# Kernel tuning notes

Hardware: AMD Instinct MI355X
Metric: run time of the kernel (lower is better)

The kernel has to match this reference:

```python
import jax, jax.numpy as jnp
import numpy as np

EMB_DIM = 1024
NUM_HEADS = 16
HEAD_DIM = EMB_DIM // NUM_HEADS
SEQ_LEN = 2048
BATCH = 2


def setup_inputs() -> dict:
    key = jax.random.key(0)
    k1, k2, k3 = jax.random.split(key, 3)
    scale = 1.0 / np.sqrt(EMB_DIM)
    x = jax.random.normal(k1, (BATCH, SEQ_LEN, EMB_DIM), dtype=jnp.float32)
    w_qkv = jax.random.normal(k2, (EMB_DIM, 3 * EMB_DIM), dtype=jnp.float32) * scale
    w_proj = jax.random.normal(k3, (EMB_DIM, EMB_DIM), dtype=jnp.float32) * scale
    b_proj = jnp.zeros((EMB_DIM,), dtype=jnp.float32)
    return {"x": x, "w_qkv": w_qkv, "w_proj": w_proj, "b_proj": b_proj}


def reference(x, w_qkv, w_proj, b_proj):
    B, T, E = x.shape
    qkv = x @ w_qkv                                   # [B, T, 3E]
    q, k, v = jnp.split(qkv, 3, axis=-1)
    # -> [B, H, T, D]
    def heads(t):
        return t.reshape(B, T, NUM_HEADS, HEAD_DIM).transpose(0, 2, 1, 3)
    q, k, v = heads(q), heads(k), heads(v)
    att = jnp.einsum("bhqd,bhkd->bhqk", q, k) / np.sqrt(HEAD_DIM).astype(x.dtype)
    causal = jnp.tril(jnp.ones((T, T), dtype=bool))   # True = keep
    att = jnp.where(causal, att, jnp.array(-jnp.inf, dtype=att.dtype))
    att = jax.nn.softmax(att, axis=-1)
    out = jnp.einsum("bhqk,bhkd->bhqd", att, v)       # [B, H, T, D]
    out = out.transpose(0, 2, 1, 3).reshape(B, T, E)
    return out @ w_proj + b_proj
```

## Files before the change

kernel.cpp:

```cpp
#include <hip/hip_runtime.h>

typedef __bf16 bf16x8 __attribute__((ext_vector_type(8)));
typedef __bf16 bf16x4 __attribute__((ext_vector_type(4)));
typedef float  f32x4  __attribute__((ext_vector_type(4)));
typedef float  f32x16 __attribute__((ext_vector_type(16)));
typedef unsigned u32x2 __attribute__((ext_vector_type(2)));
typedef unsigned u32x4 __attribute__((ext_vector_type(4)));

#define T_SEQ 2048
#define NH    16
#define HD    64
#define EMB   1024
#define BATCH 2
#define QSCALE 0.18033688f

__device__ __forceinline__ void gload_lds16(const void* g, void* lds) {
  __builtin_amdgcn_global_load_lds(
      (__attribute__((address_space(1))) void*)(g),
      (__attribute__((address_space(3))) void*)(lds), 16, 0, 0);
}

__device__ __forceinline__ f32x16 mfma32(bf16x8 a, bf16x8 b, f32x16 c) {
  return __builtin_amdgcn_mfma_f32_32x32x16_bf16(a, b, c, 0, 0, 0);
}

__device__ __forceinline__ f32x4 mfma16(bf16x8 a, bf16x8 b, f32x4 c) {
  return __builtin_amdgcn_mfma_f32_16x16x32_bf16(a, b, c, 0, 0, 0);
}

__device__ __forceinline__ unsigned cvtpk(float lo, float hi) {
  unsigned short a = __builtin_bit_cast(unsigned short, (__bf16)lo);
  unsigned short b = __builtin_bit_cast(unsigned short, (__bf16)hi);
  return (unsigned)a | ((unsigned)b << 16);
}

__global__ __launch_bounds__(256) void cvt_bf16(const float* __restrict__ in,
                                                __bf16* __restrict__ out, int n) {
  int i = (blockIdx.x * 256 + threadIdx.x) * 8;
  if (i >= n) return;
  f32x4 a = *(const f32x4*)(in + i);
  f32x4 b = *(const f32x4*)(in + i + 4);
  bf16x8 v;
  v[0] = (__bf16)a[0]; v[1] = (__bf16)a[1]; v[2] = (__bf16)a[2]; v[3] = (__bf16)a[3];
  v[4] = (__bf16)b[0]; v[5] = (__bf16)b[1]; v[6] = (__bf16)b[2]; v[7] = (__bf16)b[3];
  *(bf16x8*)(out + i) = v;
}

__global__ __launch_bounds__(256) void transpose_cvt(const float* __restrict__ in,
                                                     __bf16* __restrict__ out,
                                                     int rows, int cols) {
  __shared__ float tile[32][33];
  int c0 = blockIdx.x * 32, r0 = blockIdx.y * 32;
  int tx = threadIdx.x & 31, ty = threadIdx.x >> 5;
#pragma unroll
  for (int j = 0; j < 32; j += 8)
    tile[ty + j][tx] = in[(size_t)(r0 + ty + j) * cols + c0 + tx];
  __syncthreads();
#pragma unroll
  for (int j = 0; j < 32; j += 8)
    out[(size_t)(c0 + ty + j) * rows + r0 + tx] = (__bf16)tile[tx][ty + j];
}

template <int MODE>
__global__ __launch_bounds__(256) void gemm_bt(
    const __bf16* __restrict__ A, const __bf16* __restrict__ Bt, int K,
    __bf16* __restrict__ Qo, __bf16* __restrict__ Ko, __bf16* __restrict__ Vt,
    const float* __restrict__ bias, float* __restrict__ Cout) {
  __shared__ alignas(16) __bf16 sA[3][128 * 32];
  __shared__ alignas(16) __bf16 sB[3][128 * 32];
  const int tid = threadIdx.x;
  const int w = tid >> 6, l = tid & 63;
  const int m0 = blockIdx.y * 128, n0 = blockIdx.x * 128;
  const int lc = l & 15, lu = l >> 4;
  const int mw = (w >> 1) * 64, nw = (w & 1) * 64;
  const int rA = l >> 2;
  const int usw = (((l & 3) ^ ((rA >> 1) & 3))) * 8;
  const int rsw = (lu ^ ((lc >> 1) & 3)) * 8;

  f32x4 acc[4][4] = {};

  auto stage = [&](int buf, int kt) {
#pragma unroll
    for (int i = 0; i < 2; ++i) {
      int rr = (w * 2 + i) * 16;
      gload_lds16(A  + (size_t)(m0 + rr + rA) * K + kt + usw, &sA[buf][rr * 32]);
      gload_lds16(Bt + (size_t)(n0 + rr + rA) * K + kt + usw, &sB[buf][rr * 32]);
    }
  };

  const int NT = K >> 5;
  stage(0, 0);
  stage(1, 32);

  int bi = 0;
  for (int i = 0; i < NT; ++i) {
    if (i == NT - 1) { asm volatile("s_waitcnt vmcnt(0)" ::: "memory"); }
    else             { asm volatile("s_waitcnt vmcnt(4)" ::: "memory"); }
    __builtin_amdgcn_s_barrier();
    __builtin_amdgcn_sched_barrier(0);

    if (i + 2 < NT) {
      int bs = bi + 2; if (bs >= 3) bs -= 3;
      stage(bs, (i + 2) * 32);
    }

    bf16x8 af[4], bfr[4];
#pragma unroll
    for (int f = 0; f < 4; ++f) {
      af[f]  = *(const bf16x8*)(&sA[bi][(mw + f * 16 + lc) * 32 + rsw]);
      bfr[f] = *(const bf16x8*)(&sB[bi][(nw + f * 16 + lc) * 32 + rsw]);
    }
#pragma unroll
    for (int mf = 0; mf < 4; ++mf)
#pragma unroll
      for (int nf = 0; nf < 4; ++nf)
        acc[mf][nf] = mfma16(af[mf], bfr[nf], acc[mf][nf]);

    if (++bi >= 3) bi = 0;
  }

#pragma unroll
  for (int mf = 0; mf < 4; ++mf) {
#pragma unroll
    for (int nf = 0; nf < 4; ++nf) {
#pragma unroll
      for (int r = 0; r < 4; ++r) {
        int mg = m0 + mw + mf * 16 + lu * 4 + r;
        int ng = n0 + nw + nf * 16 + lc;
        float v = acc[mf][nf][r];
        if (MODE == 0) {
          int part = ng >> 10;
          int h = (ng >> 6) & 15;
          int d = ng & 63;
          int b = mg >> 11;
          int t = mg & 2047;
          if (part == 0) {
            Qo[(((size_t)(b * NH + h)) * T_SEQ + t) * HD + d] = (__bf16)(v * QSCALE);
          } else if (part == 1) {
            Ko[(((size_t)(b * NH + h)) * T_SEQ + t) * HD + d] = (__bf16)v;
          } else {
            Vt[(((size_t)(b * NH + h)) * HD + d) * T_SEQ + t] = (__bf16)v;
          }
        } else {
          Cout[(size_t)mg * EMB + ng] = v + bias[ng];
        }
      }
    }
  }
}

__device__ __forceinline__ void cmask32(f32x16& s0, int k0, int hi, int q) {
#pragma unroll
  for (int r = 0; r < 16; ++r) {
    int kk = k0 + 4 * hi + (r & 3) + 8 * (r >> 2);
    if (kk > q) s0[r] = -1e30f;
  }
}

__device__ __forceinline__ void softmax_pack32(
    f32x16& s0, f32x16& o0, f32x16& o1,
    float& m, float& ls, u32x4 (&pf)[2]) {
  float mx[8];
#pragma unroll
  for (int r = 0; r < 8; ++r) mx[r] = fmaxf(s0[r], s0[r + 8]);
#pragma unroll
  for (int st = 4; st > 0; st >>= 1)
#pragma unroll
    for (int r = 0; r < 8; ++r) if (r < st) mx[r] = fmaxf(mx[r], mx[r + st]);
  float pmax = fmaxf(mx[0], __shfl_xor(mx[0], 32));
  if (!__all(pmax <= m + 8.0f)) {
    float mn = fmaxf(m, pmax);
    float al = __builtin_amdgcn_exp2f(m - mn);
    m = mn;
    ls *= al;
#pragma unroll
    for (int r = 0; r < 16; ++r) { o0[r] *= al; o1[r] *= al; }
  }
  float ps = 0.f;
  f32x16 p;
#pragma unroll
  for (int r = 0; r < 16; ++r) { p[r] = __builtin_amdgcn_exp2f(s0[r] - m); ps += p[r]; }
  ps += __shfl_xor(ps, 32);
  ls += ps;
#pragma unroll
  for (int kh = 0; kh < 2; ++kh) {
    unsigned c01 = cvtpk(p[kh * 8 + 0], p[kh * 8 + 1]);
    unsigned c23 = cvtpk(p[kh * 8 + 2], p[kh * 8 + 3]);
    unsigned c45 = cvtpk(p[kh * 8 + 4], p[kh * 8 + 5]);
    unsigned c67 = cvtpk(p[kh * 8 + 6], p[kh * 8 + 7]);
    u32x2 a = __builtin_amdgcn_permlane32_swap(c01, c45, false, false);
    u32x2 c = __builtin_amdgcn_permlane32_swap(c23, c67, false, false);
    u32x4 r; r[0] = a[0]; r[1] = c[0]; r[2] = a[1]; r[3] = c[1];
    pf[kh] = r;
  }
}

__device__ __forceinline__ void dump_state(float* mo, float* mm, int reg, int l,
                                           const f32x16& o0, const f32x16& o1,
                                           float m, float ls) {
  float* po = mo + reg * 2048 + l;
#pragma unroll
  for (int r = 0; r < 16; ++r) { po[r * 64] = o0[r]; po[(16 + r) * 64] = o1[r]; }
  mm[reg * 128 + l] = m;
  mm[reg * 128 + 64 + l] = ls;
}

__device__ __forceinline__ void merge_write(const float* mo, const float* mm,
                                            int reg, int l, int hi,
                                            const f32x16& o0, const f32x16& o1,
                                            float m, float ls,
                                            __bf16* O, size_t rowbase) {
  float m1 = mm[reg * 128 + l];
  float l1 = mm[reg * 128 + 64 + l];
  float mn = fmaxf(m, m1);
  float a0 = __builtin_amdgcn_exp2f(m - mn);
  float a1 = __builtin_amdgcn_exp2f(m1 - mn);
  float inv = 1.f / (ls * a0 + l1 * a1);
  const float* po = mo + reg * 2048 + l;
#pragma unroll
  for (int dt = 0; dt < 2; ++dt) {
    const f32x16& ov = dt ? o1 : o0;
#pragma unroll
    for (int rg = 0; rg < 4; ++rg) {
      bf16x4 vv;
#pragma unroll
      for (int j = 0; j < 4; ++j) {
        int r = rg * 4 + j;
        float oth = po[(dt * 16 + r) * 64];
        vv[j] = (__bf16)((ov[r] * a0 + oth * a1) * inv);
      }
      int d = dt * 32 + rg * 8 + 4 * hi;
      *(bf16x4*)(O + rowbase + d) = vv;
    }
  }
}

__global__ __launch_bounds__(512, 4) void attn(
    const __bf16* __restrict__ Q,
    const __bf16* __restrict__ K,
    const __bf16* __restrict__ Vt,
    __bf16* __restrict__ O) {
  __shared__ alignas(16) __bf16 sKV[8][32 * 64];
  __shared__ alignas(16) float mls[4 * 2 * 64];

  const int x = blockIdx.x, bh = blockIdx.y;
  const int tid = threadIdx.x, w = tid >> 6, l = tid & 63;
  const int lq = l & 31, hi = l >> 5;
  const int c  = w >> 2;
  const int st = (w >> 1) & 1;
  const int gc = w & 1;
  const int kind = w >> 2, sp = (w >> 1) & 1, shf = w & 1;

  const __bf16* Qh = Q + (size_t)bh * T_SEQ * HD;
  const __bf16* Kh = K + (size_t)bh * T_SEQ * HD;
  const __bf16* Vh = Vt + (size_t)bh * HD * T_SEQ;

  const int C = (c == 0) ? (31 - x) : x;
  const int q0 = C * 64 + st * 32;
  const int diagT = 2 * C + st;
  const int nsup = 32 - x;

  bf16x8 qf[4];
#pragma unroll
  for (int dc = 0; dc < 4; ++dc)
    qf[dc] = *(const bf16x8*)(Qh + (size_t)(q0 + lq) * HD + dc * 16 + hi * 8);

  f32x16 o0 = {}, o1 = {};
  float m = -1e30f, ls = 0.f;

  const int r8 = l >> 3;
  const int kswz = ((l & 7) ^ r8) * 8;
  const int r4 = l >> 2;
  const int vswz = ((l & 3) ^ (r4 & 3)) * 8;

  auto stage = [&](int buf, int ss) {
    int t = 2 * ss + sp;
    int k0s = t * 32;
    if (kind == 0) {
      __bf16* dst = &sKV[buf * 2 + sp][shf * 16 * 64];
#pragma unroll
      for (int i = 0; i < 2; ++i)
        gload_lds16(Kh + (size_t)(k0s + shf * 16 + i * 8 + r8) * HD + kswz,
                    dst + i * 512);
    } else {
      __bf16* dst = &sKV[4 + buf * 2 + sp][shf * 32 * 32];
#pragma unroll
      for (int i = 0; i < 2; ++i)
        gload_lds16(Vh + (size_t)(shf * 32 + i * 16 + r4) * T_SEQ + k0s + vswz,
                    dst + i * 512);
    }
  };

  auto kfrag = [&](const __bf16* b, int row, int u) -> bf16x8 {
    return *(const bf16x8*)(b + row * 64 + ((u ^ (row & 7)) << 3));
  };
  auto vfrag = [&](const __bf16* b, int row, int u) -> bf16x8 {
    return *(const bf16x8*)(b + row * 32 + ((u ^ (row & 3)) << 3));
  };

  stage(0, 0);
  asm volatile("s_waitcnt vmcnt(0)" ::: "memory");
  __syncthreads();

  int buf = 0;
  for (int ss = 0; ss < nsup; ++ss) {
    if (ss + 1 < nsup) stage(buf ^ 1, ss + 1);
    const int tg = 2 * ss + gc;
    if (tg <= diagT) {
      const __bf16* sKb = &sKV[buf * 2 + gc][0];
      const __bf16* sVb = &sKV[4 + buf * 2 + gc][0];
      f32x16 s = {};
#pragma unroll
      for (int dc = 0; dc < 4; ++dc)
        s = mfma32(kfrag(sKb, lq, dc * 2 + hi), qf[dc], s);
      if (tg == diagT) cmask32(s, tg * 32, hi, q0 + lq);
      u32x4 pf[2];
      softmax_pack32(s, o0, o1, m, ls, pf);
#pragma unroll
      for (int ks = 0; ks < 2; ++ks) {
        bf16x8 vf0 = vfrag(sVb, lq, ks * 2 + hi);
        bf16x8 vf1 = vfrag(sVb, 32 + lq, ks * 2 + hi);
        bf16x8 pa = __builtin_bit_cast(bf16x8, pf[ks]);
        o0 = mfma32(vf0, pa, o0);
        o1 = mfma32(vf1, pa, o1);
      }
    }
    asm volatile("s_waitcnt vmcnt(0)" ::: "memory");
    __syncthreads();
    buf ^= 1;
  }

  float* mo = (float*)&sKV[0][0];
  const int reg = c * 2 + st;
  if (gc == 1) dump_state(mo, mls, reg, l, o0, o1, m, ls);
  __syncthreads();
  if (gc == 0) {
    const int b = bh >> 4, h = bh & 15;
    size_t row = (size_t)(b * T_SEQ + q0 + lq) * EMB + h * HD;
    merge_write(mo, mls, reg, l, hi, o0, o1, m, ls, O, row);
  }
}

extern "C" void kernel_launch(void* const* d_in, const int* in_sizes, int n_in,
                              void* d_out, int out_size, void* d_ws, size_t ws_size,
                              hipStream_t stream) {
  const float* x      = (const float*)d_in[0];
  const float* w_qkv  = (const float*)d_in[1];
  const float* w_proj = (const float*)d_in[2];
  const float* b_proj = (const float*)d_in[3];
  float* out = (float*)d_out;

  char* ws = (char*)d_ws;
  __bf16* xb     = (__bf16*)(ws);
  __bf16* wqkvT  = (__bf16*)(ws + (8u  << 20));
  __bf16* wprojT = (__bf16*)(ws + (14u << 20));
  __bf16* Qw     = (__bf16*)(ws + (16u << 20));
  __bf16* Kw     = (__bf16*)(ws + (24u << 20));
  __bf16* Vw     = (__bf16*)(ws + (32u << 20));
  __bf16* Ow     = xb;

  cvt_bf16<<<2048, 256, 0, stream>>>(x, xb, 4096 * 1024);
  transpose_cvt<<<dim3(3072 / 32, 1024 / 32), 256, 0, stream>>>(w_qkv, wqkvT, 1024, 3072);
  transpose_cvt<<<dim3(1024 / 32, 1024 / 32), 256, 0, stream>>>(w_proj, wprojT, 1024, 1024);

  gemm_bt<0><<<dim3(3072 / 128, 4096 / 128), 256, 0, stream>>>(
      xb, wqkvT, 1024, Qw, Kw, Vw, nullptr, nullptr);

  attn<<<dim3(16, BATCH * NH), 512, 0, stream>>>(Qw, Kw, Vw, Ow);

  gemm_bt<1><<<dim3(1024 / 128, 4096 / 128), 256, 0, stream>>>(
      Ow, wprojT, 1024, nullptr, nullptr, nullptr, b_proj, out);
}
```

Before: 125.0 us.

## Replace LDS-staged split-KV attention with per-wave register-streamed causal attention

The attention kernel no longer stages K/V tiles into shared memory with block-wide barriers or splits the key range across wave pairs that merge through LDS. Each wave now owns one 32-row query tile and streams K and V fragments straight from global memory into registers, double-buffered across two key tiles, over the full causal range. Work is balanced by pairing tile j with tile 63-j inside a block, and launch bounds drop to two blocks per CU. This removes the barriers and the merge step, but each wave now walks twice as many key tiles serially and K/V reuse across waves relies on L1/L2 caching instead of LDS.

```diff
diff --git a/kernel.cpp b/kernel.cpp
--- a/kernel.cpp
+++ b/kernel.cpp
@@ -195,71 +195,22 @@
   }
 }
 
-__device__ __forceinline__ void dump_state(float* mo, float* mm, int reg, int l,
-                                           const f32x16& o0, const f32x16& o1,
-                                           float m, float ls) {
-  float* po = mo + reg * 2048 + l;
-#pragma unroll
-  for (int r = 0; r < 16; ++r) { po[r * 64] = o0[r]; po[(16 + r) * 64] = o1[r]; }
-  mm[reg * 128 + l] = m;
-  mm[reg * 128 + 64 + l] = ls;
-}
-
-__device__ __forceinline__ void merge_write(const float* mo, const float* mm,
-                                            int reg, int l, int hi,
-                                            const f32x16& o0, const f32x16& o1,
-                                            float m, float ls,
-                                            __bf16* O, size_t rowbase) {
-  float m1 = mm[reg * 128 + l];
-  float l1 = mm[reg * 128 + 64 + l];
-  float mn = fmaxf(m, m1);
-  float a0 = __builtin_amdgcn_exp2f(m - mn);
-  float a1 = __builtin_amdgcn_exp2f(m1 - mn);
-  float inv = 1.f / (ls * a0 + l1 * a1);
-  const float* po = mo + reg * 2048 + l;
-#pragma unroll
-  for (int dt = 0; dt < 2; ++dt) {
-    const f32x16& ov = dt ? o1 : o0;
-#pragma unroll
-    for (int rg = 0; rg < 4; ++rg) {
-      bf16x4 vv;
-#pragma unroll
-      for (int j = 0; j < 4; ++j) {
-        int r = rg * 4 + j;
-        float oth = po[(dt * 16 + r) * 64];
-        vv[j] = (__bf16)((ov[r] * a0 + oth * a1) * inv);
-      }
-      int d = dt * 32 + rg * 8 + 4 * hi;
-      *(bf16x4*)(O + rowbase + d) = vv;
-    }
-  }
-}
-
-__global__ __launch_bounds__(512, 4) void attn(
+__global__ __launch_bounds__(512, 2) void attn2(
     const __bf16* __restrict__ Q,
     const __bf16* __restrict__ K,
     const __bf16* __restrict__ Vt,
     __bf16* __restrict__ O) {
-  __shared__ alignas(16) __bf16 sKV[8][32 * 64];
-  __shared__ alignas(16) float mls[4 * 2 * 64];
-
-  const int x = blockIdx.x, bh = blockIdx.y;
+  const int bh = blockIdx.y;
   const int tid = threadIdx.x, w = tid >> 6, l = tid & 63;
   const int lq = l & 31, hi = l >> 5;
-  const int c  = w >> 2;
-  const int st = (w >> 1) & 1;
-  const int gc = w & 1;
-  const int kind = w >> 2, sp = (w >> 1) & 1, shf = w & 1;
+  const int j = blockIdx.x * 4 + (w & 3);
+  const int s = (w < 4) ? j : 63 - j;
+  const int q0 = s * 32;
 
   const __bf16* Qh = Q + (size_t)bh * T_SEQ * HD;
   const __bf16* Kh = K + (size_t)bh * T_SEQ * HD;
   const __bf16* Vh = Vt + (size_t)bh * HD * T_SEQ;
 
-  const int C = (c == 0) ? (31 - x) : x;
-  const int q0 = C * 64 + st * 32;
-  const int diagT = 2 * C + st;
-  const int nsup = 32 - x;
-
   bf16x8 qf[4];
 #pragma unroll
   for (int dc = 0; dc < 4; ++dc)
@@ -268,76 +219,67 @@
   f32x16 o0 = {}, o1 = {};
   float m = -1e30f, ls = 0.f;
 
-  const int r8 = l >> 3;
-  const int kswz = ((l & 7) ^ r8) * 8;
-  const int r4 = l >> 2;
-  const int vswz = ((l & 3) ^ (r4 & 3)) * 8;
-
-  auto stage = [&](int buf, int ss) {
-    int t = 2 * ss + sp;
-    int k0s = t * 32;
-    if (kind == 0) {
-      __bf16* dst = &sKV[buf * 2 + sp][shf * 16 * 64];
-#pragma unroll
-      for (int i = 0; i < 2; ++i)
-        gload_lds16(Kh + (size_t)(k0s + shf * 16 + i * 8 + r8) * HD + kswz,
-                    dst + i * 512);
-    } else {
-      __bf16* dst = &sKV[4 + buf * 2 + sp][shf * 32 * 32];
-#pragma unroll
-      for (int i = 0; i < 2; ++i)
-        gload_lds16(Vh + (size_t)(shf * 32 + i * 16 + r4) * T_SEQ + k0s + vswz,
-                    dst + i * 512);
-    }
-  };
-
-  auto kfrag = [&](const __bf16* b, int row, int u) -> bf16x8 {
-    return *(const bf16x8*)(b + row * 64 + ((u ^ (row & 7)) << 3));
-  };
-  auto vfrag = [&](const __bf16* b, int row, int u) -> bf16x8 {
-    return *(const bf16x8*)(b + row * 32 + ((u ^ (row & 3)) << 3));
-  };
-
-  stage(0, 0);
-  asm volatile("s_waitcnt vmcnt(0)" ::: "memory");
-  __syncthreads();
-
-  int buf = 0;
-  for (int ss = 0; ss < nsup; ++ss) {
-    if (ss + 1 < nsup) stage(buf ^ 1, ss + 1);
-    const int tg = 2 * ss + gc;
-    if (tg <= diagT) {
-      const __bf16* sKb = &sKV[buf * 2 + gc][0];
-      const __bf16* sVb = &sKV[4 + buf * 2 + gc][0];
-      f32x16 s = {};
-#pragma unroll
-      for (int dc = 0; dc < 4; ++dc)
-        s = mfma32(kfrag(sKb, lq, dc * 2 + hi), qf[dc], s);
-      if (tg == diagT) cmask32(s, tg * 32, hi, q0 + lq);
-      u32x4 pf[2];
-      softmax_pack32(s, o0, o1, m, ls, pf);
-#pragma unroll
-      for (int ks = 0; ks < 2; ++ks) {
-        bf16x8 vf0 = vfrag(sVb, lq, ks * 2 + hi);
-        bf16x8 vf1 = vfrag(sVb, 32 + lq, ks * 2 + hi);
-        bf16x8 pa = __builtin_bit_cast(bf16x8, pf[ks]);
-        o0 = mfma32(vf0, pa, o0);
-        o1 = mfma32(vf1, pa, o1);
-      }
-    }
-    asm volatile("s_waitcnt vmcnt(0)" ::: "memory");
-    __syncthreads();
-    buf ^= 1;
-  }
-
-  float* mo = (float*)&sKV[0][0];
-  const int reg = c * 2 + st;
-  if (gc == 1) dump_state(mo, mls, reg, l, o0, o1, m, ls);
-  __syncthreads();
-  if (gc == 0) {
-    const int b = bh >> 4, h = bh & 15;
-    size_t row = (size_t)(b * T_SEQ + q0 + lq) * EMB + h * HD;
-    merge_write(mo, mls, reg, l, hi, o0, o1, m, ls, O, row);
+  const __bf16* Krow  = Kh + (size_t)lq * HD + hi * 8;
+  const __bf16* Vrow0 = Vh + (size_t)lq * T_SEQ + hi * 8;
+  const __bf16* Vrow1 = Vh + (size_t)(32 + lq) * T_SEQ + hi * 8;
+
+#define LOADT(t, kf, vf)                                          \
+  {                                                               \
+    const __bf16* kp = Krow + (size_t)(t) * (32 * HD);            \
+    kf[0] = *(const bf16x8*)(kp);                                 \
+    kf[1] = *(const bf16x8*)(kp + 16);                            \
+    kf[2] = *(const bf16x8*)(kp + 32);                            \
+    kf[3] = *(const bf16x8*)(kp + 48);                            \
+    vf[0] = *(const bf16x8*)(Vrow0 + (t) * 32);                   \
+    vf[1] = *(const bf16x8*)(Vrow0 + (t) * 32 + 16);              \
+    vf[2] = *(const bf16x8*)(Vrow1 + (t) * 32);                   \
+    vf[3] = *(const bf16x8*)(Vrow1 + (t) * 32 + 16);              \
+  }
+
+#define STEP(t, kf, vf)                                           \
+  {                                                               \
+    f32x16 S = {};                                                \
+    S = mfma32(kf[0], qf[0], S);                                  \
+    S = mfma32(kf[1], qf[1], S);                                  \
+    S = mfma32(kf[2], qf[2], S);                                  \
+    S = mfma32(kf[3], qf[3], S);                                  \
+    if ((t) == s) cmask32(S, (t) * 32, hi, q0 + lq);              \
+    u32x4 pf[2];                                                  \
+    softmax_pack32(S, o0, o1, m, ls, pf);                         \
+    bf16x8 pa0 = __builtin_bit_cast(bf16x8, pf[0]);               \
+    bf16x8 pa1 = __builtin_bit_cast(bf16x8, pf[1]);               \
+    o0 = mfma32(vf[0], pa0, o0);                                  \
+    o0 = mfma32(vf[1], pa1, o0);                                  \
+    o1 = mfma32(vf[2], pa0, o1);                                  \
+    o1 = mfma32(vf[3], pa1, o1);                                  \
+  }
+
+  bf16x8 kA[4], vA[4], kB[4], vB[4];
+  LOADT(0, kA, vA);
+  for (int t = 0; t <= s; t += 2) {
+    if (t + 1 <= s) LOADT(t + 1, kB, vB);
+    STEP(t, kA, vA);
+    if (t + 1 <= s) {
+      if (t + 2 <= s) LOADT(t + 2, kA, vA);
+      STEP(t + 1, kB, vB);
+    }
+  }
+#undef LOADT
+#undef STEP
+
+  const int b = bh >> 4, h = bh & 15;
+  const float inv = 1.f / ls;
+  size_t row = (size_t)(b * T_SEQ + q0 + lq) * EMB + h * HD;
+#pragma unroll
+  for (int dt = 0; dt < 2; ++dt) {
+    const f32x16& ov = dt ? o1 : o0;
+#pragma unroll
+    for (int rg = 0; rg < 4; ++rg) {
+      bf16x4 vv;
+#pragma unroll
+      for (int jj = 0; jj < 4; ++jj) vv[jj] = (__bf16)(ov[rg * 4 + jj] * inv);
+      *(bf16x4*)(O + row + dt * 32 + rg * 8 + 4 * hi) = vv;
+    }
   }
 }
 
@@ -366,7 +308,7 @@
   gemm_bt<0><<<dim3(3072 / 128, 4096 / 128), 256, 0, stream>>>(
       xb, wqkvT, 1024, Qw, Kw, Vw, nullptr, nullptr);
 
-  attn<<<dim3(16, BATCH * NH), 512, 0, stream>>>(Qw, Kw, Vw, Ow);
+  attn2<<<dim3(8, BATCH * NH), 512, 0, stream>>>(Qw, Kw, Vw, Ow);
 
   gemm_bt<1><<<dim3(1024 / 128, 4096 / 128), 256, 0, stream>>>(
       Ow, wprojT, 1024, nullptr, nullptr, nullptr, b_proj, out);
```

After: 142.7 us. 1.14x slower.

## Restructure attention into 256-thread blocks processing paired query chunks sequentially with 128-key tiles

Applied to the files above, without the earlier changes.

The attention kernel drops from 512 to 256 threads per block. Each block now processes its two causal-balanced query chunks (31-x and x) one after the other instead of in parallel wave groups. K/V staging moves to 128-key supertiles shared by all waves, with s_setprio hints around the MFMA sections and raw s_barrier plus sched_barrier syncs. The aim is fewer staging rounds and less wasted K/V loading on the short chunk. In exchange, the two chunks are serialized within a block, which lowers per-block parallelism.

```diff
diff --git a/kernel.cpp b/kernel.cpp
--- a/kernel.cpp
+++ b/kernel.cpp
@@ -235,60 +235,40 @@
   }
 }
 
-__global__ __launch_bounds__(512, 4) void attn(
+__global__ __launch_bounds__(256) void attn(
     const __bf16* __restrict__ Q,
     const __bf16* __restrict__ K,
     const __bf16* __restrict__ Vt,
     __bf16* __restrict__ O) {
-  __shared__ alignas(16) __bf16 sKV[8][32 * 64];
-  __shared__ alignas(16) float mls[4 * 2 * 64];
+  __shared__ alignas(16) __bf16 sK[2][128 * 64];
+  __shared__ alignas(16) __bf16 sV[2][64 * 128];
+  __shared__ alignas(16) float mls[2 * 128];
 
   const int x = blockIdx.x, bh = blockIdx.y;
   const int tid = threadIdx.x, w = tid >> 6, l = tid & 63;
   const int lq = l & 31, hi = l >> 5;
-  const int c  = w >> 2;
-  const int st = (w >> 1) & 1;
-  const int gc = w & 1;
-  const int kind = w >> 2, sp = (w >> 1) & 1, shf = w & 1;
+  const int st = w >> 1, gc = w & 1;
 
   const __bf16* Qh = Q + (size_t)bh * T_SEQ * HD;
   const __bf16* Kh = K + (size_t)bh * T_SEQ * HD;
   const __bf16* Vh = Vt + (size_t)bh * HD * T_SEQ;
-
-  const int C = (c == 0) ? (31 - x) : x;
-  const int q0 = C * 64 + st * 32;
-  const int diagT = 2 * C + st;
-  const int nsup = 32 - x;
-
-  bf16x8 qf[4];
-#pragma unroll
-  for (int dc = 0; dc < 4; ++dc)
-    qf[dc] = *(const bf16x8*)(Qh + (size_t)(q0 + lq) * HD + dc * 16 + hi * 8);
-
-  f32x16 o0 = {}, o1 = {};
-  float m = -1e30f, ls = 0.f;
 
   const int r8 = l >> 3;
   const int kswz = ((l & 7) ^ r8) * 8;
   const int r4 = l >> 2;
   const int vswz = ((l & 3) ^ (r4 & 3)) * 8;
 
-  auto stage = [&](int buf, int ss) {
-    int t = 2 * ss + sp;
-    int k0s = t * 32;
-    if (kind == 0) {
-      __bf16* dst = &sKV[buf * 2 + sp][shf * 16 * 64];
-#pragma unroll
-      for (int i = 0; i < 2; ++i)
-        gload_lds16(Kh + (size_t)(k0s + shf * 16 + i * 8 + r8) * HD + kswz,
-                    dst + i * 512);
-    } else {
-      __bf16* dst = &sKV[4 + buf * 2 + sp][shf * 32 * 32];
-#pragma unroll
-      for (int i = 0; i < 2; ++i)
-        gload_lds16(Vh + (size_t)(shf * 32 + i * 16 + r4) * T_SEQ + k0s + vswz,
-                    dst + i * 512);
-    }
+  auto stageS = [&](int buf, int S) {
+    const int k0s = S * 128;
+#pragma unroll
+    for (int i = 0; i < 4; ++i) {
+      int rb = (w * 4 + i) * 8;
+      gload_lds16(Kh + (size_t)(k0s + rb + r8) * HD + kswz, &sK[buf][rb * 64]);
+    }
+#pragma unroll
+    for (int i = 0; i < 4; ++i)
+      gload_lds16(Vh + (size_t)(i * 16 + r4) * T_SEQ + k0s + w * 32 + vswz,
+                  &sV[buf][w * 2048 + i * 512]);
   };
 
   auto kfrag = [&](const __bf16* b, int row, int u) -> bf16x8 {
@@ -298,47 +278,73 @@
     return *(const bf16x8*)(b + row * 32 + ((u ^ (row & 3)) << 3));
   };
 
-  stage(0, 0);
-  asm volatile("s_waitcnt vmcnt(0)" ::: "memory");
-  __syncthreads();
-
-  int buf = 0;
-  for (int ss = 0; ss < nsup; ++ss) {
-    if (ss + 1 < nsup) stage(buf ^ 1, ss + 1);
-    const int tg = 2 * ss + gc;
-    if (tg <= diagT) {
-      const __bf16* sKb = &sKV[buf * 2 + gc][0];
-      const __bf16* sVb = &sKV[4 + buf * 2 + gc][0];
-      f32x16 s = {};
-#pragma unroll
-      for (int dc = 0; dc < 4; ++dc)
-        s = mfma32(kfrag(sKb, lq, dc * 2 + hi), qf[dc], s);
-      if (tg == diagT) cmask32(s, tg * 32, hi, q0 + lq);
-      u32x4 pf[2];
-      softmax_pack32(s, o0, o1, m, ls, pf);
-#pragma unroll
-      for (int ks = 0; ks < 2; ++ks) {
-        bf16x8 vf0 = vfrag(sVb, lq, ks * 2 + hi);
-        bf16x8 vf1 = vfrag(sVb, 32 + lq, ks * 2 + hi);
-        bf16x8 pa = __builtin_bit_cast(bf16x8, pf[ks]);
-        o0 = mfma32(vf0, pa, o0);
-        o1 = mfma32(vf1, pa, o1);
+  const int b_ = bh >> 4, h_ = bh & 15;
+  float* mo = (float*)&sK[0][0];
+
+  auto phase = [&](int C) {
+    const int q0 = C * 64 + st * 32;
+    const int diagT = 2 * C + st;
+    const int nsup = (2 * C + 5) >> 2;
+
+    bf16x8 qf[4];
+#pragma unroll
+    for (int dc = 0; dc < 4; ++dc)
+      qf[dc] = *(const bf16x8*)(Qh + (size_t)(q0 + lq) * HD + dc * 16 + hi * 8);
+
+    f32x16 o0 = {}, o1 = {};
+    float m = -1e30f, ls = 0.f;
+
+    stageS(0, 0);
+    asm volatile("s_waitcnt vmcnt(0)" ::: "memory");
+    __builtin_amdgcn_s_barrier();
+    __builtin_amdgcn_sched_barrier(0);
+
+    for (int S = 0; S < nsup; ++S) {
+      const int buf = S & 1;
+      if (S + 1 < nsup) stageS(buf ^ 1, S + 1);
+#pragma unroll
+      for (int j = 0; j < 2; ++j) {
+        const int tg = 4 * S + 2 * j + gc;
+        if (tg <= diagT) {
+          const __bf16* sKb = &sK[buf][(tg & 3) * 2048];
+          const __bf16* sVb = &sV[buf][(tg & 3) * 2048];
+          f32x16 s = {};
+          __builtin_amdgcn_s_setprio(1);
+#pragma unroll
+          for (int dc = 0; dc < 4; ++dc)
+            s = mfma32(kfrag(sKb, lq, dc * 2 + hi), qf[dc], s);
+          __builtin_amdgcn_s_setprio(0);
+          if (tg == diagT) cmask32(s, tg * 32, hi, q0 + lq);
+          u32x4 pf[2];
+          softmax_pack32(s, o0, o1, m, ls, pf);
+          __builtin_amdgcn_s_setprio(1);
+#pragma unroll
+          for (int ks = 0; ks < 2; ++ks) {
+            bf16x8 vf0 = vfrag(sVb, lq, ks * 2 + hi);
+            bf16x8 vf1 = vfrag(sVb, 32 + lq, ks * 2 + hi);
+            bf16x8 pa = __builtin_bit_cast(bf16x8, pf[ks]);
+            o0 = mfma32(vf0, pa, o0);
+            o1 = mfma32(vf1, pa, o1);
+          }
+          __builtin_amdgcn_s_setprio(0);
+        }
       }
-    }
-    asm volatile("s_waitcnt vmcnt(0)" ::: "memory");
+      asm volatile("s_waitcnt vmcnt(0)" ::: "memory");
+      __builtin_amdgcn_s_barrier();
+      __builtin_amdgcn_sched_barrier(0);
+    }
+
+    if (gc == 1) dump_state(mo, mls, st, l, o0, o1, m, ls);
     __syncthreads();
-    buf ^= 1;
-  }
-
-  float* mo = (float*)&sKV[0][0];
-  const int reg = c * 2 + st;
-  if (gc == 1) dump_state(mo, mls, reg, l, o0, o1, m, ls);
-  __syncthreads();
-  if (gc == 0) {
-    const int b = bh >> 4, h = bh & 15;
-    size_t row = (size_t)(b * T_SEQ + q0 + lq) * EMB + h * HD;
-    merge_write(mo, mls, reg, l, hi, o0, o1, m, ls, O, row);
-  }
+    if (gc == 0) {
+      size_t row = (size_t)(b_ * T_SEQ + q0 + lq) * EMB + h_ * HD;
+      merge_write(mo, mls, st, l, hi, o0, o1, m, ls, O, row);
+    }
+    __syncthreads();
+  };
+
+  phase(31 - x);
+  phase(x);
 }
 
 extern "C" void kernel_launch(void* const* d_in, const int* in_sizes, int n_in,
@@ -366,7 +372,7 @@
   gemm_bt<0><<<dim3(3072 / 128, 4096 / 128), 256, 0, stream>>>(
       xb, wqkvT, 1024, Qw, Kw, Vw, nullptr, nullptr);
 
-  attn<<<dim3(16, BATCH * NH), 512, 0, stream>>>(Qw, Kw, Vw, Ow);
+  attn<<<dim3(16, BATCH * NH), 256, 0, stream>>>(Qw, Kw, Vw, Ow);
 
   gemm_bt<1><<<dim3(1024 / 128, 4096 / 128), 256, 0, stream>>>(
       Ow, wprojT, 1024, nullptr, nullptr, nullptr, b_proj, out);
```

Measured after the change: 129.7 us. +3.7%, slower.
